# Optimization experiments

Hardware: AMD Instinct MI355X
Metric: run time of the kernel (lower is better)

Reference implementation:

```python
import jax, jax.numpy as jnp
import numpy as np

B, H, W, BLK = 32, 512, 512, 8
QF_MIN, QF_MAX, QF_BIAS = 2.0, 50.0, 0.0

_RGB2YCC = jnp.array([[0.299, 0.587, 0.114],
                      [-0.168736, -0.331264, 0.5],
                      [0.5, -0.418688, -0.081312]], jnp.float32)
_YCC_OFF = jnp.array([0.0, 128.0, 128.0], jnp.float32)

Y_QTB = jnp.array([16,11,10,16,24,40,51,61,12,12,14,19,26,58,60,55,14,13,16,24,40,57,69,56,
                   14,17,22,29,51,87,80,62,18,22,37,56,68,109,103,77,24,36,55,64,81,104,113,92,
                   49,64,78,87,103,121,120,101,72,92,95,98,112,100,103,99], jnp.float32).reshape(8, 8)
C_QTB = jnp.array([17,18,24,47,99,99,99,99,18,21,26,66,99,99,99,99,24,26,56,99,99,99,99,99,
                   47,66,99,99,99,99,99,99,99,99,99,99,99,99,99,99,99,99,99,99,99,99,99,99,
                   99,99,99,99,99,99,99,99,99,99,99,99,99,99,99,99], jnp.float32).reshape(8, 8)

# orthonormal 8x8 DCT-II matrix
_k = np.arange(8.0)[:, None]; _n = np.arange(8.0)[None, :]
_C = 0.5 * np.cos((2 * _n + 1) * _k * np.pi / 16.0)
_C[0] *= 1.0 / np.sqrt(2.0)
DCT_M = jnp.asarray(_C, jnp.float32)

# standard JPEG zig-zag raster order over the 64 coefficients of an 8x8 block
ZIGZAG = jnp.array([0,1,8,16,9,2,3,10,17,24,32,25,18,11,4,5,12,19,26,33,40,48,41,34,27,20,13,6,
                    7,14,21,28,35,42,49,56,57,50,43,36,29,22,15,23,30,37,44,51,58,59,52,45,38,31,
                    39,46,53,60,61,54,47,55,62,63], jnp.int32)


def hard_round(x):
    # straight-through round: forward = round(x), backward = identity
    return x + jax.lax.stop_gradient(jnp.round(x) - x)


def split_blocks(x):
    # [B,H,W] -> [B,H/8,W/8,8,8]
    b, h, w = x.shape
    return x.reshape(b, h // BLK, BLK, w // BLK, BLK).transpose(0, 1, 3, 2, 4)


def dct2d(x):
    # 2D DCT over the trailing 8x8 dims: C @ X @ C^T
    return jnp.einsum('ij,bnmjk,lk->bnmil', DCT_M, x, DCT_M)


def _norm01(e):
    mn = e.min(axis=(1, 2), keepdims=True)
    mx = e.max(axis=(1, 2), keepdims=True)
    return (e - mn) / (mx - mn + 1e-6)


def _ac_energy(d):
    # per-block log AC energy, shape [B,h8,w8]
    return jnp.log1p(jnp.sum(d * d, axis=(-2, -1)) - d[..., 0, 0] ** 2 + 1e-6)


def _forward(rgb):
    ycbcr = hard_round(jnp.einsum('bhwc,kc->bhwk', rgb, _RGB2YCC) + _YCC_OFF) - 128.0
    y_d = dct2d(split_blocks(ycbcr[..., 0]))
    cb_d = dct2d(split_blocks(ycbcr[..., 1]))
    cr_d = dct2d(split_blocks(ycbcr[..., 2]))

    # QFMapGenerator (default): per-block AC-energy rank in [0,1], upsampled to pixels
    rank = jnp.stack([_norm01(_ac_energy(y_d)),
                      _norm01(0.5 * (_ac_energy(cb_d) + _ac_energy(cr_d)))], axis=-1)  # [B,h8,w8,2]
    rank_px = jnp.repeat(jnp.repeat(rank, BLK, axis=1), BLK, axis=2)  # [B,H,W,2]

    # RankToQF
    enc_qf = jnp.clip(hard_round(QF_MIN + rank_px * (QF_MAX - QF_MIN) + QF_BIAS), QF_MIN, QF_MAX)
    y_qf_min = enc_qf[..., 0].min(axis=(1, 2), keepdims=True)
    y_qf_max = enc_qf[..., 0].max(axis=(1, 2), keepdims=True)
    c_qf_min = enc_qf[..., 1].min(axis=(1, 2), keepdims=True)
    c_qf_max = enc_qf[..., 1].max(axis=(1, 2), keepdims=True)

    # QFToScale: standard JPEG QF -> scale factor
    enc_scale = hard_round(jnp.where(enc_qf < 50.0, 5000.0 / enc_qf, 200.0 - 2.0 * enc_qf)) / 100.0

    sy = split_blocks(enc_scale[..., 0])  # [B,h8,w8,8,8]
    sc = split_blocks(enc_scale[..., 1])
    yq = hard_round(y_d / (sy * Y_QTB))
    cbq = hard_round(cb_d / (sc * C_QTB))
    crq = hard_round(cr_d / (sc * C_QTB))
    qdct = jnp.stack([yq, cbq, crq], axis=1)  # [B,3,h8,w8,8,8]

    nb = (H // BLK) * (W // BLK)
    flat = qdct.reshape(B, 3, nb, 64)
    # delta encode along the block axis
    delta = jnp.concatenate([flat[:, :, :1], flat[:, :, 1:] - flat[:, :, :-1]], axis=2)
    # zig-zag raster scan of the 64 coefficients
    zz = delta[..., ZIGZAG]
    blocks = jnp.log(jnp.abs(zz) + 1.0) / jnp.log(2.0)
    blocks = blocks.reshape(-1, 64)
    return qdct, blocks, enc_qf, enc_scale, y_qf_min, y_qf_max, c_qf_min, c_qf_max


def setup_inputs() -> dict:
    key = jax.random.key(0)
    rgb = jax.random.uniform(key, (B, H, W, 3), jnp.float32) * 255.0
    return {"rgb": rgb}


def reference(rgb):
    return _forward(rgb)
```

## Files before the change

### kernel.cpp

```cpp
#include <hip/hip_runtime.h>
#include <math.h>

#define BB 32
#define HH 512
#define WW 512
#define NB 4096
#define QD 25165824
#define PP 16777216
#define TAILOFF (2 * (size_t)QD + 2 * (size_t)PP)

constexpr int ZZc[64] = {
    0,1,8,16,9,2,3,10,17,24,32,25,18,11,4,5,12,19,26,33,40,48,41,34,27,20,13,6,
    7,14,21,28,35,42,49,56,57,50,43,36,29,22,15,23,30,37,44,51,58,59,52,45,38,31,
    39,46,53,60,61,54,47,55,62,63};
__constant__ int c_zz[64] = {
    0,1,8,16,9,2,3,10,17,24,32,25,18,11,4,5,12,19,26,33,40,48,41,34,27,20,13,6,
    7,14,21,28,35,42,49,56,57,50,43,36,29,22,15,23,30,37,44,51,58,59,52,45,38,31,
    39,46,53,60,61,54,47,55,62,63};

struct QArg { float Cf[64]; double rqY[64]; double rqC[64]; };

__device__ __forceinline__ double qf_from_rank(double r) {
    double q = rint(2.0 + r * 48.0 + 0.0);
    return fmin(fmax(q, 2.0), 50.0);
}
__device__ __forceinline__ double scale_from_qf(double qf) {
    double s = (qf < 50.0) ? (5000.0 / qf) : (200.0 - 2.0 * qf);
    return rint(s) / 100.0;
}

__device__ __forceinline__ void ycc16(const float* __restrict__ src, int p0,
                                      int* y, int* cb, int* cr) {
    float px[48];
    const float4* s4 = (const float4*)(src + (size_t)p0 * 3);
    #pragma unroll
    for (int k = 0; k < 12; ++k) ((float4*)px)[k] = s4[k];
    #pragma unroll
    for (int k = 0; k < 16; ++k) {
        double R = px[3 * k], G = px[3 * k + 1], Bv = px[3 * k + 2];
        y[k]  = (int)(rint(R * (double)0.299f     + G * (double)0.587f     + Bv * (double)0.114f)             - 128.0);
        cb[k] = (int)(rint(R * (double)-0.168736f + G * (double)-0.331264f + Bv * (double)0.5f       + 128.0) - 128.0);
        cr[k] = (int)(rint(R * (double)0.5f       + G * (double)-0.418688f + Bv * (double)-0.081312f + 128.0) - 128.0);
    }
}

__global__ __launch_bounds__(256, 4) void k_energy(const float* __restrict__ rgb,
                                                   double* __restrict__ ey,
                                                   double* __restrict__ ec) {
    __shared__ int4 part[3][8][32];
    __shared__ double ecomb[2][64];
    int b = blockIdx.x >> 6, i = blockIdx.x & 63, t = threadIdx.x;
    const float* src = rgb + (size_t)(b * HH + i * 8) * WW * 3;
    {
        int y[16], cb[16], cr[16];
        ycc16(src, t * 16, y, cb, cr);
        int s[3][2] = {{0,0},{0,0},{0,0}}, s2[3][2] = {{0,0},{0,0},{0,0}};
        #pragma unroll
        for (int k = 0; k < 16; ++k) {
            int h = k >> 3;
            s[0][h] += y[k];  s2[0][h] += y[k] * y[k];
            s[1][h] += cb[k]; s2[1][h] += cb[k] * cb[k];
            s[2][h] += cr[k]; s2[2][h] += cr[k] * cr[k];
        }
        int r0 = t >> 5, c = t & 31;
        #pragma unroll
        for (int ch = 0; ch < 3; ++ch)
            part[ch][r0][c] = make_int4(s[ch][0], s2[ch][0], s[ch][1], s2[ch][1]);
    }
    __syncthreads();
    int ch = t >> 6, j = t & 63;
    if (ch < 3) {
        int S = 0, S2 = 0;
        #pragma unroll
        for (int r = 0; r < 8; ++r) {
            const int2* p = (const int2*)&part[ch][r][j >> 1];
            int2 v = p[j & 1];
            S += v.x; S2 += v.y;
        }
        double e = log1p((double)S2 - (double)S * (double)S * (1.0 / 64.0) + 1e-6);
        if (ch == 0) ey[b * NB + i * 64 + j] = e;
        else ecomb[ch - 1][j] = e;
    }
    __syncthreads();
    if (t < 64) ec[b * NB + i * 64 + t] = 0.5 * (ecomb[0][t] + ecomb[1][t]);
}

__global__ __launch_bounds__(256) void k_minmax(const double* __restrict__ ey,
                                                const double* __restrict__ ec,
                                                double* __restrict__ mm,
                                                float* __restrict__ out_tail) {
    __shared__ double s0[256], s1[256], s2[256], s3[256];
    int b = blockIdx.x, tid = threadIdx.x;
    double mny = 1e300, mxy = -1e300, mnc = 1e300, mxc = -1e300;
    for (int n = tid; n < NB; n += 256) {
        double vy = ey[b * NB + n], vc = ec[b * NB + n];
        mny = fmin(mny, vy); mxy = fmax(mxy, vy);
        mnc = fmin(mnc, vc); mxc = fmax(mxc, vc);
    }
    s0[tid] = mny; s1[tid] = mxy; s2[tid] = mnc; s3[tid] = mxc;
    __syncthreads();
    for (int off = 128; off > 0; off >>= 1) {
        if (tid < off) {
            s0[tid] = fmin(s0[tid], s0[tid + off]);
            s1[tid] = fmax(s1[tid], s1[tid + off]);
            s2[tid] = fmin(s2[tid], s2[tid + off]);
            s3[tid] = fmax(s3[tid], s3[tid + off]);
        }
        __syncthreads();
    }
    if (tid == 0) {
        mm[b] = s0[0]; mm[32 + b] = s1[0]; mm[64 + b] = s2[0]; mm[96 + b] = s3[0];
        double ry = (s1[0] - s0[0]) / (s1[0] - s0[0] + 1e-6);
        double rc = (s3[0] - s2[0]) / (s3[0] - s2[0] + 1e-6);
        out_tail[b]      = (float)qf_from_rank(0.0);
        out_tail[32 + b] = (float)qf_from_rank(ry);
        out_tail[64 + b] = (float)qf_from_rank(0.0);
        out_tail[96 + b] = (float)qf_from_rank(rc);
    }
}

__global__ __launch_bounds__(256, 4) void k_quant(const float* __restrict__ rgb,
                                                  QArg A,
                                                  const double* __restrict__ ey,
                                                  const double* __restrict__ ec,
                                                  const double* __restrict__ mm,
                                                  float* __restrict__ out) {
    __shared__ __align__(16) short sm[13056];
    int b = blockIdx.x >> 6, i = blockIdx.x & 63, t = threadIdx.x;
    {
        int y[16], cb[16], cr[16];
        ycc16(rgb + (size_t)(b * HH + i * 8) * WW * 3, t * 16, y, cb, cr);
        alignas(16) short yb[16], cbb[16], crb[16];
        #pragma unroll
        for (int k = 0; k < 16; ++k) {
            yb[k] = (short)y[k]; cbb[k] = (short)cb[k]; crb[k] = (short)cr[k];
        }
        int4* d0 = (int4*)&sm[0 * 4096 + 16 * t];
        int4* d1 = (int4*)&sm[1 * 4096 + 16 * t];
        int4* d2 = (int4*)&sm[2 * 4096 + 16 * t];
        d0[0] = ((int4*)yb)[0];  d0[1] = ((int4*)yb)[1];
        d1[0] = ((int4*)cbb)[0]; d1[1] = ((int4*)cbb)[1];
        d2[0] = ((int4*)crb)[0]; d2[1] = ((int4*)crb)[1];
    }
    __syncthreads();
    int ch = t >> 6, j = t & 63;
    float U[8][8];
    double qy = 0, qc = 0, sy = 1, sc = 1;
    if (ch < 3) {
        int gt = b * NB + i * 64 + j;
        double eyv = ey[gt], ecv = ec[gt];
        double mny = mm[b], mxy = mm[32 + b], mnc = mm[64 + b], mxc = mm[96 + b];
        double ry = (eyv - mny) / (mxy - mny + 1e-6);
        double rc = (ecv - mnc) / (mxc - mnc + 1e-6);
        qy = qf_from_rank(ry); qc = qf_from_rank(rc);
        sy = scale_from_qf(qy); sc = scale_from_qf(qc);
        #pragma unroll
        for (int r = 0; r < 8; ++r) {
            alignas(16) short xs[8];
            *(int4*)xs = *(const int4*)&sm[ch * 4096 + r * 512 + j * 8];
            float xr[8];
            #pragma unroll
            for (int s = 0; s < 8; ++s) xr[s] = (float)xs[s];
            #pragma unroll
            for (int v = 0; v < 8; ++v) {
                float u = 0.0f;
                #pragma unroll
                for (int s = 0; s < 8; ++s) u += xr[s] * A.Cf[v * 8 + s];
                U[r][v] = u;
            }
        }
    }
    __syncthreads();
    if (ch < 3) {
        double rinv = 1.0 / ((ch == 0) ? sy : sc);
        const double* rqt = (ch == 0) ? A.rqY : A.rqC;
        size_t qbase = (((size_t)b * 3 + ch) * NB + (size_t)(i * 64 + j)) * 64;
        int sqb = (ch * 64 + j) * 66;
        #pragma unroll
        for (int u = 0; u < 8; ++u) {
            alignas(16) float orow[8];
            alignas(4) short srow[8];
            #pragma unroll
            for (int v = 0; v < 8; ++v) {
                float d = 0.0f;
                #pragma unroll
                for (int r = 0; r < 8; ++r) d += A.Cf[u * 8 + r] * U[r][v];
                float qv = (float)rint((double)d * (rqt[u * 8 + v] * rinv));
                orow[v] = qv; srow[v] = (short)qv;
            }
            *(float4*)(out + qbase + u * 8)     = ((float4*)orow)[0];
            *(float4*)(out + qbase + u * 8 + 4) = ((float4*)orow)[1];
            short2* sd = (short2*)&sm[sqb + u * 8];
            sd[0] = ((short2*)srow)[0]; sd[1] = ((short2*)srow)[1];
            sd[2] = ((short2*)srow)[2]; sd[3] = ((short2*)srow)[3];
        }
    }
    __syncthreads();
    if (ch < 3) {
        int sqb = (ch * 64 + j) * 66;
        size_t bbase = (size_t)QD + (((size_t)b * 3 + ch) * NB + (size_t)(i * 64 + j)) * 64;
        #pragma unroll
        for (int u = 0; u < 8; ++u) {
            alignas(16) float bo[8];
            #pragma unroll
            for (int e = 0; e < 8; ++e) {
                int zk = ZZc[u * 8 + e];
                float cur = (float)sm[sqb + zk];
                float prv = (j > 0) ? (float)sm[sqb - 66 + zk] : 0.0f;
                bo[e] = log2f(fabsf(cur - prv) + 1.0f);
            }
            *(float4*)(out + bbase + u * 8)     = ((float4*)bo)[0];
            *(float4*)(out + bbase + u * 8 + 4) = ((float4*)bo)[1];
        }
        if (ch < 2) {
            float4 v4 = (ch == 0)
                ? make_float4((float)qy, (float)qc, (float)qy, (float)qc)
                : make_float4((float)sy, (float)sc, (float)sy, (float)sc);
            float* mbase = out + 2 * (size_t)QD + (ch ? PP : 0);
            size_t P = (size_t)(b * HH + i * 8) * WW + j * 8;
            #pragma unroll
            for (int rr = 0; rr < 8; ++rr) {
                float4* dst = (float4*)((float2*)mbase + P + (size_t)rr * WW);
                dst[0] = v4; dst[1] = v4; dst[2] = v4; dst[3] = v4;
            }
        }
    }
}

__global__ __launch_bounds__(256) void k_fix(const float* __restrict__ q,
                                             float* __restrict__ ob) {
    int idx = blockIdx.x * 256 + threadIdx.x;
    int rid = idx >> 6, k = idx & 63;
    int bch = rid >> 6;
    int i = rid & 63;
    size_t base = ((size_t)bch * NB + (size_t)i * 64) * 64;
    float cur = q[base + c_zz[k]];
    float prv = (i > 0) ? q[base - 64 + c_zz[k]] : 0.0f;
    ob[base + k] = log2f(fabsf(cur - prv) + 1.0f);
}

extern "C" void kernel_launch(void* const* d_in, const int* in_sizes, int n_in,
                              void* d_out, int out_size, void* d_ws, size_t ws_size,
                              hipStream_t stream) {
    const float* rgb = (const float*)d_in[0];
    float* out = (float*)d_out;
    double* ws = (double*)d_ws;
    double* ey = ws;
    double* ec = ws + (size_t)BB * NB;
    double* mm = ws + 2 * (size_t)BB * NB;

    static const double YQ[64] = {
        16,11,10,16,24,40,51,61, 12,12,14,19,26,58,60,55, 14,13,16,24,40,57,69,56,
        14,17,22,29,51,87,80,62, 18,22,37,56,68,109,103,77, 24,36,55,64,81,104,113,92,
        49,64,78,87,103,121,120,101, 72,92,95,98,112,100,103,99};
    static const double CQ[64] = {
        17,18,24,47,99,99,99,99, 18,21,26,66,99,99,99,99, 24,26,56,99,99,99,99,99,
        47,66,99,99,99,99,99,99, 99,99,99,99,99,99,99,99, 99,99,99,99,99,99,99,99,
        99,99,99,99,99,99,99,99, 99,99,99,99,99,99,99,99};

    QArg qa;
    for (int k = 0; k < 8; ++k)
        for (int n = 0; n < 8; ++n) {
            double v = 0.5 * cos((2.0 * n + 1.0) * (double)k * M_PI / 16.0);
            if (k == 0) v *= 0.70710678118654752440;
            qa.Cf[k * 8 + n] = (float)v;
        }
    for (int k = 0; k < 64; ++k) { qa.rqY[k] = 1.0 / YQ[k]; qa.rqC[k] = 1.0 / CQ[k]; }

    dim3 blk(256);
    k_energy<<<BB * 64, blk, 0, stream>>>(rgb, ey, ec);
    k_minmax<<<BB, blk, 0, stream>>>(ey, ec, mm, out + TAILOFF);
    k_quant<<<BB * 64, blk, 0, stream>>>(rgb, qa, ey, ec, mm, out);
    k_fix<<<(BB * 3 * 64 * 64) / 256, blk, 0, stream>>>(out, out + QD);
}
```

Baseline: 499.2 us.

## Replace shared-memory delta staging with packed registers and wavefront shuffles

Quantized coefficients are now packed as int16 pairs in 32 registers per thread, and the previous block's values come from a wavefront __shfl_up instead of a round trip through LDS. This removes two __syncthreads barriers and the shared-memory writes and reads of the quantized blocks, and shrinks the shared allocation. It costs more registers and 32 shuffles per thread. Lane 0 of each 64-wide wave gets the neighbour from outside the row, which matches the old j>0 case only if k_fix later corrects those entries.

Measured after the change: 599.8 us. 20.2% more time.

```diff
diff --git a/kernel.cpp b/kernel.cpp
--- a/kernel.cpp
+++ b/kernel.cpp
@@ -125,7 +125,7 @@
                                                   const double* __restrict__ ec,
                                                   const double* __restrict__ mm,
                                                   float* __restrict__ out) {
-    __shared__ __align__(16) short sm[13056];
+    __shared__ __align__(16) short sm[12288];
     int b = blockIdx.x >> 6, i = blockIdx.x & 63, t = threadIdx.x;
     {
         int y[16], cb[16], cr[16];
@@ -144,16 +144,16 @@
     }
     __syncthreads();
     int ch = t >> 6, j = t & 63;
-    float U[8][8];
-    double qy = 0, qc = 0, sy = 1, sc = 1;
     if (ch < 3) {
         int gt = b * NB + i * 64 + j;
         double eyv = ey[gt], ecv = ec[gt];
         double mny = mm[b], mxy = mm[32 + b], mnc = mm[64 + b], mxc = mm[96 + b];
         double ry = (eyv - mny) / (mxy - mny + 1e-6);
         double rc = (ecv - mnc) / (mxc - mnc + 1e-6);
-        qy = qf_from_rank(ry); qc = qf_from_rank(rc);
-        sy = scale_from_qf(qy); sc = scale_from_qf(qc);
+        double qy = qf_from_rank(ry), qc = qf_from_rank(rc);
+        double sy = scale_from_qf(qy), sc = scale_from_qf(qc);
+
+        float U[8][8];
         #pragma unroll
         for (int r = 0; r < 8; ++r) {
             alignas(16) short xs[8];
@@ -169,48 +169,44 @@
                 U[r][v] = u;
             }
         }
-    }
-    __syncthreads();
-    if (ch < 3) {
         double rinv = 1.0 / ((ch == 0) ? sy : sc);
         const double* rqt = (ch == 0) ? A.rqY : A.rqC;
         size_t qbase = (((size_t)b * 3 + ch) * NB + (size_t)(i * 64 + j)) * 64;
-        int sqb = (ch * 64 + j) * 66;
+        int qp[32];
         #pragma unroll
         for (int u = 0; u < 8; ++u) {
             alignas(16) float orow[8];
-            alignas(4) short srow[8];
             #pragma unroll
             for (int v = 0; v < 8; ++v) {
                 float d = 0.0f;
                 #pragma unroll
                 for (int r = 0; r < 8; ++r) d += A.Cf[u * 8 + r] * U[r][v];
-                float qv = (float)rint((double)d * (rqt[u * 8 + v] * rinv));
-                orow[v] = qv; srow[v] = (short)qv;
+                orow[v] = (float)rint((double)d * (rqt[u * 8 + v] * rinv));
             }
             *(float4*)(out + qbase + u * 8)     = ((float4*)orow)[0];
             *(float4*)(out + qbase + u * 8 + 4) = ((float4*)orow)[1];
-            short2* sd = (short2*)&sm[sqb + u * 8];
-            sd[0] = ((short2*)srow)[0]; sd[1] = ((short2*)srow)[1];
-            sd[2] = ((short2*)srow)[2]; sd[3] = ((short2*)srow)[3];
-        }
-    }
-    __syncthreads();
-    if (ch < 3) {
-        int sqb = (ch * 64 + j) * 66;
-        size_t bbase = (size_t)QD + (((size_t)b * 3 + ch) * NB + (size_t)(i * 64 + j)) * 64;
-        #pragma unroll
-        for (int u = 0; u < 8; ++u) {
-            alignas(16) float bo[8];
-            #pragma unroll
-            for (int e = 0; e < 8; ++e) {
-                int zk = ZZc[u * 8 + e];
-                float cur = (float)sm[sqb + zk];
-                float prv = (j > 0) ? (float)sm[sqb - 66 + zk] : 0.0f;
-                bo[e] = log2f(fabsf(cur - prv) + 1.0f);
-            }
-            *(float4*)(out + bbase + u * 8)     = ((float4*)bo)[0];
-            *(float4*)(out + bbase + u * 8 + 4) = ((float4*)bo)[1];
+            #pragma unroll
+            for (int h = 0; h < 4; ++h) {
+                int s0 = (int)orow[2 * h], s1 = (int)orow[2 * h + 1];
+                qp[u * 4 + h] = (s0 & 0xffff) | (int)(((unsigned)s1) << 16);
+            }
+        }
+        int pp[32];
+        #pragma unroll
+        for (int w = 0; w < 32; ++w) pp[w] = __shfl_up(qp[w], 1, 64);
+        size_t bbase = (size_t)QD + qbase;
+        #pragma unroll
+        for (int g = 0; g < 16; ++g) {
+            alignas(16) float bo[4];
+            #pragma unroll
+            for (int q = 0; q < 4; ++q) {
+                constexpr int dummy = 0; (void)dummy;
+                int m = ZZc[g * 4 + q];
+                int cu = (m & 1) ? (qp[m >> 1] >> 16) : ((qp[m >> 1] << 16) >> 16);
+                int pv = (m & 1) ? (pp[m >> 1] >> 16) : ((pp[m >> 1] << 16) >> 16);
+                bo[q] = log2f(fabsf((float)(cu - pv)) + 1.0f);
+            }
+            *(float4*)(out + bbase + g * 4) = ((float4*)bo)[0];
         }
         if (ch < 2) {
             float4 v4 = (ch == 0)
@@ -234,8 +230,9 @@
     int bch = rid >> 6;
     int i = rid & 63;
     size_t base = ((size_t)bch * NB + (size_t)i * 64) * 64;
-    float cur = q[base + c_zz[k]];
-    float prv = (i > 0) ? q[base - 64 + c_zz[k]] : 0.0f;
+    int zk = c_zz[k];
+    float cur = q[base + zk];
+    float prv = (i > 0) ? q[base - 64 + zk] : 0.0f;
     ob[base + k] = log2f(fabsf(cur - prv) + 1.0f);
 }
 
```
